# Optimization experiments

Hardware: AMD Instinct MI355X
Metric: run time of the kernel (lower is better)

The kernel has to match this reference:

```python
import jax, jax.numpy as jnp
from jax import lax
import numpy as np

B, T, I, H, FC = 1024, 512, 16, 50, 64


def _lstm_layer(x, w_ih, w_hh, b_ih, b_hh):
    """PyTorch-semantics single LSTM layer, batch_first. x: [B,T,in]. Returns h-seq [B,T,H]."""
    b = x.shape[0]
    h_dim = w_hh.shape[1]
    # Precompute input contribution for all timesteps in one big GEMM: [B,T,4H]
    gates_x = jnp.einsum('bti,gi->btg', x, w_ih) + b_ih + b_hh

    def step(carry, gx):
        h, c = carry
        g = gx + h @ w_hh.T                      # [B,4H]; gate order i,f,g,o (PyTorch)
        i_g, f_g, g_g, o_g = jnp.split(g, 4, axis=-1)
        i_g = jax.nn.sigmoid(i_g)
        f_g = jax.nn.sigmoid(f_g)
        g_g = jnp.tanh(g_g)
        o_g = jax.nn.sigmoid(o_g)
        c = f_g * c + i_g * g_g
        h = o_g * jnp.tanh(c)
        return (h, c), h

    h0 = jnp.zeros((b, h_dim), x.dtype)
    (_, _), hs = lax.scan(step, (h0, h0), jnp.swapaxes(gates_x, 0, 1))  # time-major scan
    return jnp.swapaxes(hs, 0, 1)


def setup_inputs() -> dict:
    key = jax.random.key(0)
    ks = jax.random.split(key, 14)
    s_i = 1.0 / np.sqrt(H)  # PyTorch LSTM init: U(-1/sqrt(H), 1/sqrt(H))
    u = lambda k, shape, s: jax.random.uniform(k, shape, jnp.float32, -s, s)
    return {
        'x': jax.random.normal(ks[0], (B, T, I), jnp.float32),
        'w_ih0': u(ks[1], (4 * H, I), s_i),
        'w_hh0': u(ks[2], (4 * H, H), s_i),
        'b_ih0': u(ks[3], (4 * H,), s_i),
        'b_hh0': u(ks[4], (4 * H,), s_i),
        'w_ih1': u(ks[5], (4 * H, H), s_i),
        'w_hh1': u(ks[6], (4 * H, H), s_i),
        'b_ih1': u(ks[7], (4 * H,), s_i),
        'b_hh1': u(ks[8], (4 * H,), s_i),
        'fc1_w': u(ks[9], (FC, H), 1.0 / np.sqrt(H)),
        'fc1_b': u(ks[10], (FC,), 1.0 / np.sqrt(H)),
        'fc2_w': u(ks[11], (1, FC), 1.0 / np.sqrt(FC)),
        'fc2_b': u(ks[12], (1,), 1.0 / np.sqrt(FC)),
    }


def reference(x, w_ih0, w_hh0, b_ih0, b_hh0, w_ih1, w_hh1, b_ih1, b_hh1,
              fc1_w, fc1_b, fc2_w, fc2_b):
    h1 = _lstm_layer(x, w_ih0, w_hh0, b_ih0, b_hh0)    # [B,T,H]
    h2 = _lstm_layer(h1, w_ih1, w_hh1, b_ih1, b_hh1)   # [B,T,H]
    last = h2[:, -1, :]                                 # [B,H]
    hidden = jax.nn.relu(last @ fc1_w.T + fc1_b)        # dropout is identity at inference
    return hidden @ fc2_w.T + fc2_b                     # [B,1]
```

## Files before the change

### kernel.cpp

```cpp
#include <hip/hip_runtime.h>

#define B_    1024
#define T_    512
#define I_    16
#define H_    50
#define FC_   64
#define HALFW 28
#define HP    56
#define R_    2

typedef float v2f __attribute__((ext_vector_type(2)));

__device__ __forceinline__ float frcp(float x)   { return __builtin_amdgcn_rcpf(x); }
__device__ __forceinline__ float sigm(float x)   { return frcp(1.0f + __expf(-x)); }
__device__ __forceinline__ float tanh_f(float x) { return 1.0f - 2.0f * frcp(1.0f + __expf(2.0f * x)); }
__device__ __forceinline__ v2f   mk2(float a, float b) { v2f r; r.x = a; r.y = b; return r; }

__device__ __forceinline__ v2f pk_fma(v2f a, v2f b, v2f acc) {
    asm("v_pk_fma_f32 %0, %1, %2, %0" : "+v"(acc) : "v"(a), "v"(b));
    return acc;
}

__device__ __forceinline__ float dpp_xor1(float v) {
    return __int_as_float(__builtin_amdgcn_update_dpp(0, __float_as_int(v), 0xB1, 0xF, 0xF, true));
}
__device__ __forceinline__ float dpp_xor2(float v) {
    return __int_as_float(__builtin_amdgcn_update_dpp(0, __float_as_int(v), 0x4E, 0xF, 0xF, true));
}

#define PKDOT(acc, W, kk, hv) { acc = pk_fma(W[2*(kk)],   mk2(hv.x, hv.y), acc); \
                                acc = pk_fma(W[2*(kk)+1], mk2(hv.z, hv.w), acc); }
#define XDOT(acc, Wj, v0, v1) { acc = pk_fma(Wj[0], mk2(v0.x, v0.y), acc); \
                                acc = pk_fma(Wj[1], mk2(v0.z, v0.w), acc); \
                                acc = pk_fma(Wj[2], mk2(v1.x, v1.y), acc); \
                                acc = pk_fma(Wj[3], mk2(v1.z, v1.w), acc); }

__global__ __launch_bounds__(512) __attribute__((amdgpu_waves_per_eu(2, 4)))
void lstm_pipe3(
    const float* __restrict__ x,
    const float* __restrict__ w_ih0, const float* __restrict__ w_hh0,
    const float* __restrict__ b_ih0, const float* __restrict__ b_hh0,
    const float* __restrict__ w_ih1, const float* __restrict__ w_hh1,
    const float* __restrict__ b_ih1, const float* __restrict__ b_hh1,
    const float* __restrict__ fc1_w, const float* __restrict__ fc1_b,
    const float* __restrict__ fc2_w, const float* __restrict__ fc2_b,
    float* __restrict__ out)
{
    __shared__ float h0s[2][R_][HP];
    __shared__ float h1s[2][R_][HP];

    const int tid  = threadIdx.x;
    const int team = tid >> 8;
    const int lt   = tid & 255;
    const int u    = lt >> 2;
    const int qp   = (lt >> 1) & 1;
    const int s    = lt & 1;
    const bool gl  = lt < 4 * H_;
    const int row0 = blockIdx.x * R_;

    const float qa = qp ? 2.0f : -1.0f;
    const float qb = qp ? 1.0f :  0.0f;
    const float qm = qp ? -2.0f : 1.0f;

    v2f wX[2][14], wY[2][14];
    float bias[2] = {0.f, 0.f};
    if (gl) {
        #pragma unroll
        for (int j = 0; j < 2; ++j) {
            const int g = (2 * qp + j) * H_ + u;
            if (team == 0) {
                #pragma unroll
                for (int k = 0; k < 14; ++k) {
                    const int j0 = s * HALFW + 2 * k, j1 = j0 + 1;
                    wX[j][k] = mk2(j0 < H_ ? w_hh0[g * H_ + j0] : 0.f,
                                   j1 < H_ ? w_hh0[g * H_ + j1] : 0.f);
                }
                #pragma unroll
                for (int k = 0; k < 4; ++k)
                    wY[j][k] = mk2(w_ih0[g * I_ + s * 8 + 2 * k],
                                   w_ih0[g * I_ + s * 8 + 2 * k + 1]);
                if (s == 0) bias[j] = b_ih0[g] + b_hh0[g];
            } else {
                #pragma unroll
                for (int k = 0; k < 14; ++k) {
                    const int j0 = s * HALFW + 2 * k, j1 = j0 + 1;
                    wX[j][k] = mk2(j0 < H_ ? w_ih1[g * H_ + j0] : 0.f,
                                   j1 < H_ ? w_ih1[g * H_ + j1] : 0.f);
                    wY[j][k] = mk2(j0 < H_ ? w_hh1[g * H_ + j0] : 0.f,
                                   j1 < H_ ? w_hh1[g * H_ + j1] : 0.f);
                }
                if (s == 0) bias[j] = b_ih1[g] + b_hh1[g];
            }
        }
    }

    if (tid < 2 * R_ * HP) { ((float*)h0s)[tid] = 0.f; ((float*)h1s)[tid] = 0.f; }
    float c[R_] = {0.f, 0.f};
    __syncthreads();

    auto cell = [&](v2f P0, v2f P1, float& cc) -> float {
        float p0 = P0.x + P0.y;  p0 += dpp_xor1(p0);
        float p1 = P1.x + P1.y;  p1 += dpp_xor1(p1);
        float act0 = qb + qm * frcp(1.0f + __expf(qa * p0));
        float act1 = sigm(p1);
        float ox0 = dpp_xor2(act0);
        float ox1 = dpp_xor2(act1);
        float gi = qp ? ox0 : act0;
        float gf = qp ? ox1 : act1;
        float gg = qp ? act0 : ox0;
        float go = qp ? act1 : ox1;
        cc = gf * cc + gi * gg;
        return go * tanh_f(cc);
    };

    #pragma unroll 2
    for (int t = 0; t < T_; ++t) {
        const int pp = t & 1;
        if (team == 0) {
            if (gl) {
                float4 xv[R_][2];
                #pragma unroll
                for (int r = 0; r < R_; ++r) {
                    const float* xp = x + ((size_t)(row0 + r) * T_ + t) * I_ + s * 8;
                    xv[r][0] = *(const float4*)xp;
                    xv[r][1] = *(const float4*)(xp + 4);
                }
                v2f P0[R_], P1[R_];
                #pragma unroll
                for (int r = 0; r < R_; ++r) {
                    const float4* hp = (const float4*)(&h0s[pp][r][s * HALFW]);
                    P0[r] = mk2(bias[0], 0.f); P1[r] = mk2(bias[1], 0.f);
                    #pragma unroll
                    for (int k = 0; k < 7; ++k) {
                        float4 hv = hp[k];
                        PKDOT(P0[r], wX[0], k, hv); PKDOT(P1[r], wX[1], k, hv);
                    }
                }
                #pragma unroll
                for (int r = 0; r < R_; ++r) {
                    XDOT(P0[r], wY[0], xv[r][0], xv[r][1]);
                    XDOT(P1[r], wY[1], xv[r][0], xv[r][1]);
                    float hv = cell(P0[r], P1[r], c[r]);
                    if ((lt & 3) == 0) h0s[pp ^ 1][r][u] = hv;
                }
            }
        } else {
            if (gl && t > 0) {
                #pragma unroll
                for (int r = 0; r < R_; ++r) {
                    const float4* h0p = (const float4*)(&h0s[pp][r][s * HALFW]);
                    const float4* h1p = (const float4*)(&h1s[pp][r][s * HALFW]);
                    v2f P0 = mk2(bias[0], 0.f), P1 = mk2(bias[1], 0.f);
                    #pragma unroll
                    for (int k = 0; k < 7; ++k) {
                        float4 hv = h0p[k];
                        PKDOT(P0, wX[0], k, hv); PKDOT(P1, wX[1], k, hv);
                    }
                    #pragma unroll
                    for (int k = 0; k < 7; ++k) {
                        float4 hv = h1p[k];
                        PKDOT(P0, wY[0], k, hv); PKDOT(P1, wY[1], k, hv);
                    }
                    float hv = cell(P0, P1, c[r]);
                    if ((lt & 3) == 0) h1s[pp ^ 1][r][u] = hv;
                }
            }
        }
        __syncthreads();
    }

    if (team == 1 && gl) {
        #pragma unroll
        for (int r = 0; r < R_; ++r) {
            const float4* h0p = (const float4*)(&h0s[0][r][s * HALFW]);
            const float4* h1p = (const float4*)(&h1s[0][r][s * HALFW]);
            v2f P0 = mk2(bias[0], 0.f), P1 = mk2(bias[1], 0.f);
            #pragma unroll
            for (int k = 0; k < 7; ++k) {
                float4 hv = h0p[k];
                PKDOT(P0, wX[0], k, hv); PKDOT(P1, wX[1], k, hv);
            }
            #pragma unroll
            for (int k = 0; k < 7; ++k) {
                float4 hv = h1p[k];
                PKDOT(P0, wY[0], k, hv); PKDOT(P1, wY[1], k, hv);
            }
            float hv = cell(P0, P1, c[r]);
            if ((lt & 3) == 0) h1s[1][r][u] = hv;
        }
    }
    __syncthreads();

    if (tid < R_ * FC_) {
        const int r = tid >> 6, f = tid & 63;
        const float* hf = h1s[1][r];
        float a = fc1_b[f];
        #pragma unroll
        for (int j = 0; j < H_; ++j) a += fc1_w[f * H_ + j] * hf[j];
        float v = fmaxf(a, 0.f) * fc2_w[f];
        #pragma unroll
        for (int off = 1; off < FC_; off <<= 1) v += __shfl_xor(v, off);
        if (f == 0) out[row0 + r] = v + fc2_b[0];
    }
}

extern "C" void kernel_launch(void* const* d_in, const int* in_sizes, int n_in,
                              void* d_out, int out_size, void* d_ws, size_t ws_size,
                              hipStream_t stream) {
    const float* x     = (const float*)d_in[0];
    const float* w_ih0 = (const float*)d_in[1];
    const float* w_hh0 = (const float*)d_in[2];
    const float* b_ih0 = (const float*)d_in[3];
    const float* b_hh0 = (const float*)d_in[4];
    const float* w_ih1 = (const float*)d_in[5];
    const float* w_hh1 = (const float*)d_in[6];
    const float* b_ih1 = (const float*)d_in[7];
    const float* b_hh1 = (const float*)d_in[8];
    const float* fc1_w = (const float*)d_in[9];
    const float* fc1_b = (const float*)d_in[10];
    const float* fc2_w = (const float*)d_in[11];
    const float* fc2_b = (const float*)d_in[12];
    float* out = (float*)d_out;

    dim3 grid(B_ / R_), block(512);
    hipLaunchKernelGGL(lstm_pipe3, grid, block, 0, stream,
                       x, w_ih0, w_hh0, b_ih0, b_hh0,
                       w_ih1, w_hh1, b_ih1, b_hh1,
                       fc1_w, fc1_b, fc2_w, fc2_b, out);
}
```

Baseline: 1.024 ms.

## Process four batch rows per block and prefetch x into LDS via team-1 staging

Doubles the rows handled per block from 2 to 4, halving the grid to 256 blocks so each block amortizes weight registers over more rows. The layer-0 team no longer loads x from global memory on its critical path. Idle team-1 lanes prefetch x two steps ahead into a 4-slot LDS ring. It also adds s_setprio around the compute sections and tightens waves_per_eu to 2. The risks are longer per-step serial work per block and fewer blocks to fill the 256 CUs.

```diff
diff --git a/kernel.cpp b/kernel.cpp
--- a/kernel.cpp
+++ b/kernel.cpp
@@ -7,7 +7,7 @@
 #define FC_   64
 #define HALFW 28
 #define HP    56
-#define R_    2
+#define R_    4
 
 typedef float v2f __attribute__((ext_vector_type(2)));
 
@@ -35,8 +35,8 @@
                                 acc = pk_fma(Wj[2], mk2(v1.x, v1.y), acc); \
                                 acc = pk_fma(Wj[3], mk2(v1.z, v1.w), acc); }
 
-__global__ __launch_bounds__(512) __attribute__((amdgpu_waves_per_eu(2, 4)))
-void lstm_pipe3(
+__global__ __launch_bounds__(512) __attribute__((amdgpu_waves_per_eu(2, 2)))
+void lstm_pipe4(
     const float* __restrict__ x,
     const float* __restrict__ w_ih0, const float* __restrict__ w_hh0,
     const float* __restrict__ b_ih0, const float* __restrict__ b_hh0,
@@ -48,6 +48,7 @@
 {
     __shared__ float h0s[2][R_][HP];
     __shared__ float h1s[2][R_][HP];
+    __shared__ float xs[4][R_ * I_];
 
     const int tid  = threadIdx.x;
     const int team = tid >> 8;
@@ -95,7 +96,16 @@
     }
 
     if (tid < 2 * R_ * HP) { ((float*)h0s)[tid] = 0.f; ((float*)h1s)[tid] = 0.f; }
-    float c[R_] = {0.f, 0.f};
+
+    const bool stg = (team == 1) && (lt < R_ * I_);
+    const float* sbase = nullptr;
+    float x_pend = 0.f;
+    if (stg) {
+        sbase = x + (size_t)(row0 + (lt >> 4)) * T_ * I_ + (lt & 15);
+        xs[0][lt] = sbase[0];
+        x_pend = sbase[(size_t)1 * I_];
+    }
+    float c[R_] = {0.f, 0.f, 0.f, 0.f};
     __syncthreads();
 
     auto cell = [&](v2f P0, v2f P1, float& cc) -> float {
@@ -116,36 +126,35 @@
     #pragma unroll 2
     for (int t = 0; t < T_; ++t) {
         const int pp = t & 1;
+        if (stg) {
+            xs[(t + 1) & 3][lt] = x_pend;
+            const int ts = (t + 2 < T_) ? (t + 2) : (T_ - 1);
+            x_pend = sbase[(size_t)ts * I_];
+        }
         if (team == 0) {
             if (gl) {
-                float4 xv[R_][2];
-                #pragma unroll
-                for (int r = 0; r < R_; ++r) {
-                    const float* xp = x + ((size_t)(row0 + r) * T_ + t) * I_ + s * 8;
-                    xv[r][0] = *(const float4*)xp;
-                    xv[r][1] = *(const float4*)(xp + 4);
-                }
-                v2f P0[R_], P1[R_];
+                __builtin_amdgcn_s_setprio(1);
                 #pragma unroll
                 for (int r = 0; r < R_; ++r) {
                     const float4* hp = (const float4*)(&h0s[pp][r][s * HALFW]);
-                    P0[r] = mk2(bias[0], 0.f); P1[r] = mk2(bias[1], 0.f);
+                    const float4* xp = (const float4*)(&xs[t & 3][r * I_ + s * 8]);
+                    v2f P0 = mk2(bias[0], 0.f), P1 = mk2(bias[1], 0.f);
+                    const float4 xv0 = xp[0], xv1 = xp[1];
                     #pragma unroll
                     for (int k = 0; k < 7; ++k) {
                         float4 hv = hp[k];
-                        PKDOT(P0[r], wX[0], k, hv); PKDOT(P1[r], wX[1], k, hv);
+                        PKDOT(P0, wX[0], k, hv); PKDOT(P1, wX[1], k, hv);
                     }
-                }
-                #pragma unroll
-                for (int r = 0; r < R_; ++r) {
-                    XDOT(P0[r], wY[0], xv[r][0], xv[r][1]);
-                    XDOT(P1[r], wY[1], xv[r][0], xv[r][1]);
-                    float hv = cell(P0[r], P1[r], c[r]);
+                    XDOT(P0, wY[0], xv0, xv1);
+                    XDOT(P1, wY[1], xv0, xv1);
+                    float hv = cell(P0, P1, c[r]);
                     if ((lt & 3) == 0) h0s[pp ^ 1][r][u] = hv;
                 }
+                __builtin_amdgcn_s_setprio(0);
             }
         } else {
             if (gl && t > 0) {
+                __builtin_amdgcn_s_setprio(1);
                 #pragma unroll
                 for (int r = 0; r < R_; ++r) {
                     const float4* h0p = (const float4*)(&h0s[pp][r][s * HALFW]);
@@ -164,6 +173,7 @@
                     float hv = cell(P0, P1, c[r]);
                     if ((lt & 3) == 0) h1s[pp ^ 1][r][u] = hv;
                 }
+                __builtin_amdgcn_s_setprio(0);
             }
         }
         __syncthreads();
@@ -223,7 +233,7 @@
     float* out = (float*)d_out;
 
     dim3 grid(B_ / R_), block(512);
-    hipLaunchKernelGGL(lstm_pipe3, grid, block, 0, stream,
+    hipLaunchKernelGGL(lstm_pipe4, grid, block, 0, stream,
                        x, w_ih0, w_hh0, b_ih0, b_hh0,
                        w_ih1, w_hh1, b_ih1, b_hh1,
                        fc1_w, fc1_b, fc2_w, fc2_b, out);
```

Result: no change. 1.017 ms (-0.7%).
